# Kernel optimization log

Hardware: AMD Instinct MI355X
Metric: run time of the kernel (lower is better)

## Reference

```python
import jax, jax.numpy as jnp
import numpy as np

B, S, E, H = 8, 2048, 1024, 64

def setup_inputs() -> dict:
    key = jax.random.key(0)
    ks = jax.random.split(key, 10)
    inp = {
        'input_Q': jax.random.normal(ks[0], (B, S, E), dtype=jnp.float32),
        'input_K': jax.random.normal(ks[1], (B, S, E), dtype=jnp.float32),
        'input_V': jax.random.normal(ks[2], (B, S, E), dtype=jnp.float32),
        'mask': jax.random.randint(ks[3], (B, S, S), 0, 2) > 0,
        # Linear params: torch Linear(E, H) -> weight [H, E], use as x @ W^T + b; store transposed [E, H]
        'Wq': jax.random.normal(ks[4], (E, H), dtype=jnp.float32) / np.sqrt(E),
        'bq': jnp.zeros((H,), dtype=jnp.float32),
        'Wk': jax.random.normal(ks[5], (E, H), dtype=jnp.float32) / np.sqrt(E),
        'bk': jnp.zeros((H,), dtype=jnp.float32),
        'Wv': jax.random.normal(ks[6], (E, H), dtype=jnp.float32) / np.sqrt(E),
        'bv': jnp.zeros((H,), dtype=jnp.float32),
    }
    return inp

def reference(input_Q, input_K, input_V, mask, Wq, bq, Wk, bk, Wv, bv):
    Q = jnp.einsum('bse,eh->bsh', input_Q, Wq) + bq  # [B,S,H]
    K = jnp.einsum('bse,eh->bsh', input_K, Wk) + bk
    V = jnp.einsum('bse,eh->bsh', input_V, Wv) + bv
    scores = jnp.einsum('bqh,bkh->bqk', Q, K) / np.sqrt(H).astype(np.float32)  # [B,S,S]
    # faithful to masked_fill_(mask, 1e-10) BEFORE softmax
    scores = jnp.where(mask, jnp.float32(1e-10), scores)
    attn = jax.nn.softmax(scores, axis=-1)
    # dropout is identity in eval/reference mode
    return jnp.einsum('bqk,bkh->bqh', attn, V)
```

## Files before the change

kernel.cpp:

```cpp
#include <hip/hip_runtime.h>
#include <hip/hip_bf16.h>
#include <stdint.h>

constexpr int Bc = 8, Sc = 2048, Ec = 1024, Hc = 64;

typedef __bf16 bf16x8 __attribute__((ext_vector_type(8)));
typedef float f32x4 __attribute__((ext_vector_type(4)));
typedef unsigned short ushort8 __attribute__((ext_vector_type(8)));
typedef unsigned short ushort4v __attribute__((ext_vector_type(4)));
typedef uint32_t uint32x4 __attribute__((ext_vector_type(4)));

static __device__ __forceinline__ unsigned short f2bf(float f) {
  uint32_t u = __builtin_bit_cast(uint32_t, f);
  u = u + 0x7fffu + ((u >> 16) & 1u);
  return (unsigned short)(u >> 16);
}
static __device__ __forceinline__ bf16x8 ldb8(const unsigned short* p) {
  return __builtin_bit_cast(bf16x8, *(const ushort8*)p);
}
static __device__ __forceinline__ uint32_t pk2bf(float a, float b) {
  return (uint32_t)f2bf(a) | ((uint32_t)f2bf(b) << 16);
}

__global__ __launch_bounds__(256) void wt_kernel(
    const float* __restrict__ Wq, const float* __restrict__ Wk,
    const float* __restrict__ Wv, unsigned short* __restrict__ Wt) {
  int idx = blockIdx.x * 256 + threadIdx.x;
  int m = idx >> 16;
  int r = idx & 65535;
  int h = r >> 10;
  int e = r & 1023;
  const float* W = (m == 0) ? Wq : (m == 1) ? Wk : Wv;
  float scale = (m == 0) ? 0.125f : 1.0f;
  Wt[idx] = f2bf(W[e * Hc + h] * scale);
}

__global__ __launch_bounds__(256) void mask_kernel(
    const int* __restrict__ mask, uint32_t* __restrict__ Mb) {
  int w = blockIdx.x * 256 + threadIdx.x;
  const int* src = mask + (size_t)w * 32;
  uint32_t bits = 0;
#pragma unroll
  for (int i = 0; i < 8; i++) {
    int4 v = *(const int4*)(src + i * 4);
    bits |= (v.x ? 1u : 0u) << (i * 4 + 0);
    bits |= (v.y ? 1u : 0u) << (i * 4 + 1);
    bits |= (v.z ? 1u : 0u) << (i * 4 + 2);
    bits |= (v.w ? 1u : 0u) << (i * 4 + 3);
  }
  Mb[w] = bits;
}

__global__ __launch_bounds__(256, 5) void proj_kernel(
    const float* __restrict__ Xq, const float* __restrict__ Xk,
    const float* __restrict__ Xv, const float* __restrict__ bq,
    const float* __restrict__ bk, const float* __restrict__ bv,
    const unsigned short* __restrict__ Wt,
    unsigned short* __restrict__ Qb, unsigned short* __restrict__ Kb,
    unsigned short* __restrict__ Vt) {
  const int mat = blockIdx.y;
  const float* X = (mat == 0) ? Xq : (mat == 1) ? Xk : Xv;
  const float* bias = (mat == 0) ? bq : (mat == 1) ? bk : bv;
  const float bscale = (mat == 0) ? 0.125f : 1.0f;
  const unsigned short* W = Wt + mat * (Hc * Ec);

  const int tid = threadIdx.x;
  const int wave = tid >> 6, lane = tid & 63;
  const int rl = lane & 15, kg = lane >> 4;
  const int row0 = blockIdx.x * 16;
  const int kw = wave * 256;

  __shared__ __align__(16) char smem[32768];

  const float* xsrc = X + (size_t)row0 * Ec;
#pragma unroll
  for (int i = 0; i < 16; i++) {
    int idx = i * 256 + tid;
    float4 v = *(const float4*)(xsrc + (size_t)idx * 4);
    int f = idx * 4;
    int row = f >> 10, col = f & 1023;
    uint32_t byte = (uint32_t)(row * 2048 + col * 2) ^ (uint32_t)((row & 7) << 4);
    uint2 pk;
    pk.x = pk2bf(v.x, v.y);
    pk.y = pk2bf(v.z, v.w);
    *(uint2*)(smem + byte) = pk;
  }
  __syncthreads();

  const unsigned short* wp0 = W + (size_t)(0 * 16 + rl) * Ec + kw + kg * 8;
  const unsigned short* wp1 = W + (size_t)(1 * 16 + rl) * Ec + kw + kg * 8;
  const unsigned short* wp2 = W + (size_t)(2 * 16 + rl) * Ec + kw + kg * 8;
  const unsigned short* wp3 = W + (size_t)(3 * 16 + rl) * Ec + kw + kg * 8;

  f32x4 acc[4];
#pragma unroll
  for (int nt = 0; nt < 4; nt++) acc[nt] = (f32x4){0.f, 0.f, 0.f, 0.f};

#pragma unroll
  for (int c = 0; c < 8; c++) {
    int col = kw + kg * 8 + c * 32;
    uint32_t byte = (uint32_t)(rl * 2048 + col * 2) ^ (uint32_t)((rl & 7) << 4);
    bf16x8 aX = *(const bf16x8*)(smem + byte);
    ushort8 w0 = *(const ushort8*)(wp0 + c * 32);
    ushort8 w1 = *(const ushort8*)(wp1 + c * 32);
    ushort8 w2 = *(const ushort8*)(wp2 + c * 32);
    ushort8 w3 = *(const ushort8*)(wp3 + c * 32);
    acc[0] = __builtin_amdgcn_mfma_f32_16x16x32_bf16(
        aX, __builtin_bit_cast(bf16x8, w0), acc[0], 0, 0, 0);
    acc[1] = __builtin_amdgcn_mfma_f32_16x16x32_bf16(
        aX, __builtin_bit_cast(bf16x8, w1), acc[1], 0, 0, 0);
    acc[2] = __builtin_amdgcn_mfma_f32_16x16x32_bf16(
        aX, __builtin_bit_cast(bf16x8, w2), acc[2], 0, 0, 0);
    acc[3] = __builtin_amdgcn_mfma_f32_16x16x32_bf16(
        aX, __builtin_bit_cast(bf16x8, w3), acc[3], 0, 0, 0);
  }

  __syncthreads();
  float (*slab)[16][64] = (float (*)[16][64])smem;
#pragma unroll
  for (int nt = 0; nt < 4; nt++)
#pragma unroll
    for (int r = 0; r < 4; r++)
      slab[wave][kg * 4 + r][nt * 16 + rl] = acc[nt][r];
  __syncthreads();

  if (mat < 2) {
    unsigned short* out = (mat == 0) ? Qb : Kb;
    int row = wave * 4 + (lane >> 4);
    int col0 = (lane & 15) * 4;
    f32x4 s0 = *(const f32x4*)&slab[0][row][col0];
    f32x4 s1 = *(const f32x4*)&slab[1][row][col0];
    f32x4 s2 = *(const f32x4*)&slab[2][row][col0];
    f32x4 s3 = *(const f32x4*)&slab[3][row][col0];
    float4 bv4 = *(const float4*)(bias + col0);
    f32x4 v = s0 + s1 + s2 + s3;
    v[0] += bv4.x * bscale; v[1] += bv4.y * bscale;
    v[2] += bv4.z * bscale; v[3] += bv4.w * bscale;
    ushort4v o;
#pragma unroll
    for (int i = 0; i < 4; i++) o[i] = f2bf(v[i]);
    *(ushort4v*)(out + (size_t)(row0 + row) * Hc + col0) = o;
  } else {
    int h = lane;
    int bb = row0 >> 11;
    int sbase = (row0 & 2047) + wave * 4;
    float bh = bias[h];
    ushort4v o;
#pragma unroll
    for (int r = 0; r < 4; r++) {
      float v = slab[0][wave * 4 + r][h] + slab[1][wave * 4 + r][h] +
                slab[2][wave * 4 + r][h] + slab[3][wave * 4 + r][h] + bh;
      o[r] = f2bf(v);
    }
    *(ushort4v*)(Vt + ((size_t)bb * Hc + h) * Sc + sbase) = o;
  }
}

__global__ __launch_bounds__(256, 4) void attn_kernel(
    const unsigned short* __restrict__ Qb, const unsigned short* __restrict__ Kb,
    const unsigned short* __restrict__ Vt, const uint32_t* __restrict__ Mb,
    float* __restrict__ out) {
  const int id = blockIdx.x;
  const int b = id & 7;
  const int q0 = (id >> 3) * 16;
  const int tid = threadIdx.x;
  const int wave = tid >> 6, lane = tid & 63;
  const int rl = lane & 15;

  __shared__ unsigned short Ps[4][16][72];
  __shared__ float sm[4][16], sl[4][16];
  __shared__ float Os[4][16][64];

  const unsigned short* qptr =
      Qb + ((size_t)b * Sc + q0 + rl) * Hc + (lane >> 4) * 8;
  bf16x8 aQ0 = ldb8(qptr);
  bf16x8 aQ1 = ldb8(qptr + 32);

  float m_r[4], l_r[4];
  f32x4 Oacc[4];
#pragma unroll
  for (int r = 0; r < 4; r++) { m_r[r] = -INFINITY; l_r[r] = 0.f; }
#pragma unroll
  for (int ht = 0; ht < 4; ht++) Oacc[ht] = (f32x4){0.f, 0.f, 0.f, 0.f};

  const uint32_t* mbase[4];
#pragma unroll
  for (int r = 0; r < 4; r++)
    mbase[r] = Mb + ((size_t)b * Sc + q0 + (lane >> 4) * 4 + r) * 64;

  const unsigned short* kbase =
      Kb + ((size_t)b * Sc) * Hc + (size_t)rl * Hc + (lane >> 4) * 8;
  const unsigned short* vbase[4];
#pragma unroll
  for (int ht = 0; ht < 4; ht++)
    vbase[ht] = Vt + ((size_t)b * Hc + ht * 16 + rl) * Sc + (lane >> 4) * 8;

  const int kw = wave * 512;
  uint2 mva[4], mvb[4];

  auto issue_mask = [&](int koff, uint2 (&mv)[4]) {
#pragma unroll
    for (int r = 0; r < 4; r++)
      mv[r] = *(const uint2*)(mbase[r] + (koff >> 5));
  };
  auto compress = [&](const uint2 (&mv)[4]) -> uint32_t {
    uint32_t bits = 0;
#pragma unroll
    for (int r = 0; r < 4; r++) {
      bits |= ((mv[r].x >> rl) & 1u) << (0 + r);
      bits |= ((mv[r].x >> (16 + rl)) & 1u) << (4 + r);
      bits |= ((mv[r].y >> rl) & 1u) << (8 + r);
      bits |= ((mv[r].y >> (16 + rl)) & 1u) << (12 + r);
    }
    return bits;
  };

  auto process = [&](int koff, uint32_t bits) {
    float sv[4][4];
#pragma unroll
    for (int nt = 0; nt < 4; nt++) {
      const unsigned short* kp = kbase + (size_t)(koff + nt * 16) * Hc;
      bf16x8 bK0 = ldb8(kp);
      bf16x8 bK1 = ldb8(kp + 32);
      f32x4 s = (f32x4){0.f, 0.f, 0.f, 0.f};
      s = __builtin_amdgcn_mfma_f32_16x16x32_bf16(aQ0, bK0, s, 0, 0, 0);
      s = __builtin_amdgcn_mfma_f32_16x16x32_bf16(aQ1, bK1, s, 0, 0, 0);
#pragma unroll
      for (int r = 0; r < 4; r++)
        sv[nt][r] = ((bits >> (nt * 4 + r)) & 1u) ? 1e-10f : s[r];
    }

    float rmax[4];
#pragma unroll
    for (int r = 0; r < 4; r++) {
      rmax[r] = fmaxf(fmaxf(sv[0][r], sv[1][r]), fmaxf(sv[2][r], sv[3][r]));
#pragma unroll
      for (int off = 1; off < 16; off <<= 1)
        rmax[r] = fmaxf(rmax[r], __shfl_xor(rmax[r], off, 64));
    }

    float alpha[4], p[4][4], psum[4];
#pragma unroll
    for (int r = 0; r < 4; r++) {
      float mnew = fmaxf(m_r[r], rmax[r]);
      alpha[r] = __expf(m_r[r] - mnew);
      m_r[r] = mnew;
      psum[r] = 0.f;
    }
#pragma unroll
    for (int nt = 0; nt < 4; nt++)
#pragma unroll
      for (int r = 0; r < 4; r++) {
        p[nt][r] = __expf(sv[nt][r] - m_r[r]);
        psum[r] += p[nt][r];
      }
#pragma unroll
    for (int r = 0; r < 4; r++) {
#pragma unroll
      for (int off = 1; off < 16; off <<= 1)
        psum[r] += __shfl_xor(psum[r], off, 64);
      l_r[r] = l_r[r] * alpha[r] + psum[r];
    }
#pragma unroll
    for (int ht = 0; ht < 4; ht++)
#pragma unroll
      for (int r = 0; r < 4; r++) Oacc[ht][r] *= alpha[r];

#pragma unroll
    for (int nt = 0; nt < 4; nt++)
#pragma unroll
      for (int r = 0; r < 4; r++)
        Ps[wave][(lane >> 4) * 4 + r][nt * 16 + rl] = f2bf(p[nt][r]);

#pragma unroll
    for (int ks = 0; ks < 2; ks++) {
      bf16x8 aP = ldb8(&Ps[wave][rl][ks * 32 + (lane >> 4) * 8]);
#pragma unroll
      for (int ht = 0; ht < 4; ht++) {
        bf16x8 bV = ldb8(vbase[ht] + koff + ks * 32);
        Oacc[ht] = __builtin_amdgcn_mfma_f32_16x16x32_bf16(aP, bV, Oacc[ht], 0, 0, 0);
      }
    }
  };

  issue_mask(kw, mva);
  for (int c2 = 0; c2 < 8; c2 += 2) {
    issue_mask(kw + (c2 + 1) * 64, mvb);
    process(kw + c2 * 64, compress(mva));
    if (c2 + 2 < 8) issue_mask(kw + (c2 + 2) * 64, mva);
    process(kw + (c2 + 1) * 64, compress(mvb));
  }

  if (rl == 0) {
#pragma unroll
    for (int r = 0; r < 4; r++) {
      sm[wave][(lane >> 4) * 4 + r] = m_r[r];
      sl[wave][(lane >> 4) * 4 + r] = l_r[r];
    }
  }
  __syncthreads();

  float coef[4];
#pragma unroll
  for (int r = 0; r < 4; r++) {
    int row = (lane >> 4) * 4 + r;
    float M = fmaxf(fmaxf(sm[0][row], sm[1][row]), fmaxf(sm[2][row], sm[3][row]));
    coef[r] = __expf(m_r[r] - M);
  }
#pragma unroll
  for (int ht = 0; ht < 4; ht++)
#pragma unroll
    for (int r = 0; r < 4; r++)
      Os[wave][(lane >> 4) * 4 + r][ht * 16 + rl] = Oacc[ht][r] * coef[r];
  __syncthreads();

  {
#pragma unroll
    for (int i = 0; i < 4; i++) {
      int row = wave * 4 + i;
      float M = fmaxf(fmaxf(sm[0][row], sm[1][row]), fmaxf(sm[2][row], sm[3][row]));
      float L = sl[0][row] * __expf(sm[0][row] - M) +
                sl[1][row] * __expf(sm[1][row] - M) +
                sl[2][row] * __expf(sm[2][row] - M) +
                sl[3][row] * __expf(sm[3][row] - M);
      float acc = Os[0][row][lane] + Os[1][row][lane] +
                  Os[2][row][lane] + Os[3][row][lane];
      out[((size_t)b * Sc + q0 + row) * Hc + lane] = acc / L;
    }
  }
}

extern "C" void kernel_launch(void* const* d_in, const int* in_sizes, int n_in,
                              void* d_out, int out_size, void* d_ws, size_t ws_size,
                              hipStream_t stream) {
  const float* Xq = (const float*)d_in[0];
  const float* Xk = (const float*)d_in[1];
  const float* Xv = (const float*)d_in[2];
  const int* mask = (const int*)d_in[3];
  const float* Wq = (const float*)d_in[4];
  const float* bq = (const float*)d_in[5];
  const float* Wk = (const float*)d_in[6];
  const float* bk = (const float*)d_in[7];
  const float* Wv = (const float*)d_in[8];
  const float* bv = (const float*)d_in[9];

  unsigned short* Qb = (unsigned short*)d_ws;
  unsigned short* Kb = Qb + (size_t)Bc * Sc * Hc;
  unsigned short* Vt = Kb + (size_t)Bc * Sc * Hc;
  unsigned short* Wt = Vt + (size_t)Bc * Sc * Hc;
  uint32_t* Mb = (uint32_t*)(Wt + (size_t)3 * Hc * Ec);

  wt_kernel<<<dim3(3 * Hc * Ec / 256), 256, 0, stream>>>(Wq, Wk, Wv, Wt);
  mask_kernel<<<dim3(Bc * Sc * (Sc / 32) / 256), 256, 0, stream>>>(mask, Mb);
  proj_kernel<<<dim3(Bc * Sc / 16, 3), 256, 0, stream>>>(Xq, Xk, Xv, bq, bk, bv,
                                                         Wt, Qb, Kb, Vt);
  attn_kernel<<<dim3(Bc * Sc / 16), 256, 0, stream>>>(Qb, Kb, Vt, Mb,
                                                      (float*)d_out);
}
```

Baseline: 424.3 us.

## Pipeline projection X loads via direct global-to-LDS double buffering

Rewrites the projection kernel so each block processes 64 rows as four 16-row slabs. Raw fp32 X is streamed directly into LDS with global_load_lds in a double-buffered pipeline, and the bf16 conversion moves into the compute step. Each wave now owns 16 output columns over the full K dimension, which removes the cross-wave LDS reduction. The cost is a smaller grid, 64KB of LDS per block, and hand-placed waitcnt/barrier synchronisation that is fragile.

```diff
diff --git a/kernel.cpp b/kernel.cpp
--- a/kernel.cpp
+++ b/kernel.cpp
@@ -21,6 +21,11 @@
 static __device__ __forceinline__ uint32_t pk2bf(float a, float b) {
   return (uint32_t)f2bf(a) | ((uint32_t)f2bf(b) << 16);
 }
+
+#define GLOBAL_LOAD_LDS16(g, l)                                              \
+  __builtin_amdgcn_global_load_lds(                                          \
+      (const __attribute__((address_space(1))) void*)(g),                    \
+      (__attribute__((address_space(3))) void*)(l), 16, 0, 0)
 
 __global__ __launch_bounds__(256) void wt_kernel(
     const float* __restrict__ Wq, const float* __restrict__ Wk,
@@ -51,7 +56,7 @@
   Mb[w] = bits;
 }
 
-__global__ __launch_bounds__(256, 5) void proj_kernel(
+__global__ __launch_bounds__(256, 2) void proj_kernel(
     const float* __restrict__ Xq, const float* __restrict__ Xk,
     const float* __restrict__ Xv, const float* __restrict__ bq,
     const float* __restrict__ bk, const float* __restrict__ bv,
@@ -67,92 +72,89 @@
   const int tid = threadIdx.x;
   const int wave = tid >> 6, lane = tid & 63;
   const int rl = lane & 15, kg = lane >> 4;
-  const int row0 = blockIdx.x * 16;
-  const int kw = wave * 256;
-
-  __shared__ __align__(16) char smem[32768];
-
-  const float* xsrc = X + (size_t)row0 * Ec;
-#pragma unroll
-  for (int i = 0; i < 16; i++) {
-    int idx = i * 256 + tid;
-    float4 v = *(const float4*)(xsrc + (size_t)idx * 4);
-    int f = idx * 4;
-    int row = f >> 10, col = f & 1023;
-    uint32_t byte = (uint32_t)(row * 2048 + col * 2) ^ (uint32_t)((row & 7) << 4);
-    uint2 pk;
-    pk.x = pk2bf(v.x, v.y);
-    pk.y = pk2bf(v.z, v.w);
-    *(uint2*)(smem + byte) = pk;
-  }
-  __syncthreads();
-
-  const unsigned short* wp0 = W + (size_t)(0 * 16 + rl) * Ec + kw + kg * 8;
-  const unsigned short* wp1 = W + (size_t)(1 * 16 + rl) * Ec + kw + kg * 8;
-  const unsigned short* wp2 = W + (size_t)(2 * 16 + rl) * Ec + kw + kg * 8;
-  const unsigned short* wp3 = W + (size_t)(3 * 16 + rl) * Ec + kw + kg * 8;
-
-  f32x4 acc[4];
-#pragma unroll
-  for (int nt = 0; nt < 4; nt++) acc[nt] = (f32x4){0.f, 0.f, 0.f, 0.f};
-
-#pragma unroll
-  for (int c = 0; c < 8; c++) {
-    int col = kw + kg * 8 + c * 32;
-    uint32_t byte = (uint32_t)(rl * 2048 + col * 2) ^ (uint32_t)((rl & 7) << 4);
-    bf16x8 aX = *(const bf16x8*)(smem + byte);
-    ushort8 w0 = *(const ushort8*)(wp0 + c * 32);
-    ushort8 w1 = *(const ushort8*)(wp1 + c * 32);
-    ushort8 w2 = *(const ushort8*)(wp2 + c * 32);
-    ushort8 w3 = *(const ushort8*)(wp3 + c * 32);
-    acc[0] = __builtin_amdgcn_mfma_f32_16x16x32_bf16(
-        aX, __builtin_bit_cast(bf16x8, w0), acc[0], 0, 0, 0);
-    acc[1] = __builtin_amdgcn_mfma_f32_16x16x32_bf16(
-        aX, __builtin_bit_cast(bf16x8, w1), acc[1], 0, 0, 0);
-    acc[2] = __builtin_amdgcn_mfma_f32_16x16x32_bf16(
-        aX, __builtin_bit_cast(bf16x8, w2), acc[2], 0, 0, 0);
-    acc[3] = __builtin_amdgcn_mfma_f32_16x16x32_bf16(
-        aX, __builtin_bit_cast(bf16x8, w3), acc[3], 0, 0, 0);
-  }
-
-  __syncthreads();
-  float (*slab)[16][64] = (float (*)[16][64])smem;
-#pragma unroll
-  for (int nt = 0; nt < 4; nt++)
-#pragma unroll
-    for (int r = 0; r < 4; r++)
-      slab[wave][kg * 4 + r][nt * 16 + rl] = acc[nt][r];
-  __syncthreads();
-
-  if (mat < 2) {
-    unsigned short* out = (mat == 0) ? Qb : Kb;
-    int row = wave * 4 + (lane >> 4);
-    int col0 = (lane & 15) * 4;
-    f32x4 s0 = *(const f32x4*)&slab[0][row][col0];
-    f32x4 s1 = *(const f32x4*)&slab[1][row][col0];
-    f32x4 s2 = *(const f32x4*)&slab[2][row][col0];
-    f32x4 s3 = *(const f32x4*)&slab[3][row][col0];
-    float4 bv4 = *(const float4*)(bias + col0);
-    f32x4 v = s0 + s1 + s2 + s3;
-    v[0] += bv4.x * bscale; v[1] += bv4.y * bscale;
-    v[2] += bv4.z * bscale; v[3] += bv4.w * bscale;
-    ushort4v o;
-#pragma unroll
-    for (int i = 0; i < 4; i++) o[i] = f2bf(v[i]);
-    *(ushort4v*)(out + (size_t)(row0 + row) * Hc + col0) = o;
-  } else {
-    int h = lane;
-    int bb = row0 >> 11;
-    int sbase = (row0 & 2047) + wave * 4;
-    float bh = bias[h];
-    ushort4v o;
-#pragma unroll
-    for (int r = 0; r < 4; r++) {
-      float v = slab[0][wave * 4 + r][h] + slab[1][wave * 4 + r][h] +
-                slab[2][wave * 4 + r][h] + slab[3][wave * 4 + r][h] + bh;
-      o[r] = f2bf(v);
-    }
-    *(ushort4v*)(Vt + ((size_t)bb * Hc + h) * Sc + sbase) = o;
+
+  __shared__ __align__(16) char smem[65536];
+
+  const char* xb = (const char*)X + (size_t)blockIdx.x * 262144;
+  const unsigned short* wp_base = W + (size_t)(wave * 16 + rl) * Ec + kg * 8;
+  const float bcol = bias[wave * 16 + rl] * bscale;
+
+  auto stage = [&](int slab, int half, int buf) {
+#pragma unroll
+    for (int j = 0; j < 8; j++) {
+      int row = wave * 4 + (j >> 1);
+      int part = j & 1;
+      const char* src = xb + (size_t)slab * 65536 + row * 4096 + half * 2048 +
+                        part * 1024 + ((lane ^ (row & 7)) * 16);
+      char* dst = smem + buf * 32768 + row * 2048 + part * 1024;
+      GLOBAL_LOAD_LDS16(src, dst);
+    }
+  };
+
+  auto compute = [&](int half, int buf, f32x4& acc) {
+    const char* lb = smem + buf * 32768;
+    const unsigned short* wp = wp_base + half * 512;
+    const uint32_t sw = (uint32_t)((rl & 7) << 4);
+#pragma unroll
+    for (int c = 0; c < 16; c++) {
+      uint32_t boff = (uint32_t)(kg * 32 + c * 128);
+      float4 x0 = *(const float4*)(lb + rl * 2048 + (boff ^ sw));
+      float4 x1 = *(const float4*)(lb + rl * 2048 + ((boff + 16) ^ sw));
+      ushort8 wv = *(const ushort8*)(wp + c * 32);
+      uint32x4 u = (uint32x4){pk2bf(x0.x, x0.y), pk2bf(x0.z, x0.w),
+                              pk2bf(x1.x, x1.y), pk2bf(x1.z, x1.w)};
+      acc = __builtin_amdgcn_mfma_f32_16x16x32_bf16(
+          __builtin_bit_cast(bf16x8, u), __builtin_bit_cast(bf16x8, wv), acc,
+          0, 0, 0);
+    }
+  };
+
+  stage(0, 0, 0);
+  stage(0, 1, 1);
+
+#pragma unroll 1
+  for (int sl = 0; sl < 4; sl++) {
+    f32x4 acc = (f32x4){0.f, 0.f, 0.f, 0.f};
+
+    asm volatile("s_waitcnt vmcnt(8)" ::: "memory");
+    __builtin_amdgcn_sched_barrier(0);
+    __builtin_amdgcn_s_barrier();
+    compute(0, 0, acc);
+    asm volatile("s_waitcnt lgkmcnt(0)" ::: "memory");
+    __builtin_amdgcn_sched_barrier(0);
+    __builtin_amdgcn_s_barrier();
+    if (sl < 3) stage(sl + 1, 0, 0);
+
+    if (sl < 3)
+      asm volatile("s_waitcnt vmcnt(8)" ::: "memory");
+    else
+      asm volatile("s_waitcnt vmcnt(0)" ::: "memory");
+    __builtin_amdgcn_sched_barrier(0);
+    __builtin_amdgcn_s_barrier();
+    compute(1, 1, acc);
+
+    {
+      int rowg = blockIdx.x * 64 + sl * 16;
+      if (mat < 2) {
+        unsigned short* out = (mat == 0) ? Qb : Kb;
+#pragma unroll
+        for (int r = 0; r < 4; r++)
+          out[(size_t)(rowg + kg * 4 + r) * Hc + wave * 16 + rl] =
+              f2bf(acc[r] + bcol);
+      } else {
+        int bb = rowg >> 11;
+        int sloc = (rowg & 2047) + kg * 4;
+        ushort4v o;
+#pragma unroll
+        for (int r = 0; r < 4; r++) o[r] = f2bf(acc[r] + bcol);
+        *(ushort4v*)(Vt + ((size_t)bb * Hc + wave * 16 + rl) * Sc + sloc) = o;
+      }
+    }
+
+    asm volatile("s_waitcnt lgkmcnt(0)" ::: "memory");
+    __builtin_amdgcn_sched_barrier(0);
+    __builtin_amdgcn_s_barrier();
+    if (sl < 3) stage(sl + 1, 1, 1);
   }
 }
 
@@ -352,8 +354,8 @@
 
   wt_kernel<<<dim3(3 * Hc * Ec / 256), 256, 0, stream>>>(Wq, Wk, Wv, Wt);
   mask_kernel<<<dim3(Bc * Sc * (Sc / 32) / 256), 256, 0, stream>>>(mask, Mb);
-  proj_kernel<<<dim3(Bc * Sc / 16, 3), 256, 0, stream>>>(Xq, Xk, Xv, bq, bk, bv,
-                                                         Wt, Qb, Kb, Vt);
+  proj_kernel<<<dim3(256, 3), 256, 0, stream>>>(Xq, Xk, Xv, bq, bk, bv,
+                                                Wt, Qb, Kb, Vt);
   attn_kernel<<<dim3(Bc * Sc / 16), 256, 0, stream>>>(Qb, Kb, Vt, Mb,
                                                       (float*)d_out);
 }
```

Result: slower. 436.0 us (+2.8%).

## Prefetch K tiles across chunks, add MFMA priority hints, split projection launches

Applied to the files above, without the earlier changes.

The attention kernel now double-buffers K operand loads in registers, issuing the next chunk's K loads right after the current QK^T MFMAs so their latency overlaps the softmax work. MFMA sections are wrapped in s_setprio to favour matrix issue across waves. The projection kernel is split into three separate launches with scalar arguments instead of one 2D grid that selects pointers per block. The prefetch raises register pressure, which may lower occupancy, and the extra launches add launch overhead.

```diff
diff --git a/kernel.cpp b/kernel.cpp
--- a/kernel.cpp
+++ b/kernel.cpp
@@ -52,18 +52,9 @@
 }
 
 __global__ __launch_bounds__(256, 5) void proj_kernel(
-    const float* __restrict__ Xq, const float* __restrict__ Xk,
-    const float* __restrict__ Xv, const float* __restrict__ bq,
-    const float* __restrict__ bk, const float* __restrict__ bv,
-    const unsigned short* __restrict__ Wt,
-    unsigned short* __restrict__ Qb, unsigned short* __restrict__ Kb,
-    unsigned short* __restrict__ Vt) {
-  const int mat = blockIdx.y;
-  const float* X = (mat == 0) ? Xq : (mat == 1) ? Xk : Xv;
-  const float* bias = (mat == 0) ? bq : (mat == 1) ? bk : bv;
-  const float bscale = (mat == 0) ? 0.125f : 1.0f;
-  const unsigned short* W = Wt + mat * (Hc * Ec);
-
+    const float* __restrict__ X, const float* __restrict__ bias,
+    const unsigned short* __restrict__ W, unsigned short* __restrict__ out,
+    float bscale, int vmode) {
   const int tid = threadIdx.x;
   const int wave = tid >> 6, lane = tid & 63;
   const int rl = lane & 15, kg = lane >> 4;
@@ -124,8 +115,7 @@
       slab[wave][kg * 4 + r][nt * 16 + rl] = acc[nt][r];
   __syncthreads();
 
-  if (mat < 2) {
-    unsigned short* out = (mat == 0) ? Qb : Kb;
+  if (vmode == 0) {
     int row = wave * 4 + (lane >> 4);
     int col0 = (lane & 15) * 4;
     f32x4 s0 = *(const f32x4*)&slab[0][row][col0];
@@ -152,7 +142,7 @@
                 slab[2][wave * 4 + r][h] + slab[3][wave * 4 + r][h] + bh;
       o[r] = f2bf(v);
     }
-    *(ushort4v*)(Vt + ((size_t)bb * Hc + h) * Sc + sbase) = o;
+    *(ushort4v*)(out + ((size_t)bb * Hc + h) * Sc + sbase) = o;
   }
 }
 
@@ -197,6 +187,7 @@
 
   const int kw = wave * 512;
   uint2 mva[4], mvb[4];
+  bf16x8 kA[4][2], kB[4][2];
 
   auto issue_mask = [&](int koff, uint2 (&mv)[4]) {
 #pragma unroll
@@ -214,21 +205,31 @@
     }
     return bits;
   };
-
-  auto process = [&](int koff, uint32_t bits) {
-    float sv[4][4];
+  auto loadK = [&](int koff, bf16x8 (&kb)[4][2]) {
 #pragma unroll
     for (int nt = 0; nt < 4; nt++) {
       const unsigned short* kp = kbase + (size_t)(koff + nt * 16) * Hc;
-      bf16x8 bK0 = ldb8(kp);
-      bf16x8 bK1 = ldb8(kp + 32);
+      kb[nt][0] = ldb8(kp);
+      kb[nt][1] = ldb8(kp + 32);
+    }
+  };
+
+  auto process = [&](int koff, uint32_t bits, const bf16x8 (&kb)[4][2],
+                     bool pre, int koff_next, bf16x8 (&knext)[4][2]) {
+    float sv[4][4];
+    __builtin_amdgcn_s_setprio(1);
+#pragma unroll
+    for (int nt = 0; nt < 4; nt++) {
       f32x4 s = (f32x4){0.f, 0.f, 0.f, 0.f};
-      s = __builtin_amdgcn_mfma_f32_16x16x32_bf16(aQ0, bK0, s, 0, 0, 0);
-      s = __builtin_amdgcn_mfma_f32_16x16x32_bf16(aQ1, bK1, s, 0, 0, 0);
+      s = __builtin_amdgcn_mfma_f32_16x16x32_bf16(aQ0, kb[nt][0], s, 0, 0, 0);
+      s = __builtin_amdgcn_mfma_f32_16x16x32_bf16(aQ1, kb[nt][1], s, 0, 0, 0);
 #pragma unroll
       for (int r = 0; r < 4; r++)
         sv[nt][r] = ((bits >> (nt * 4 + r)) & 1u) ? 1e-10f : s[r];
     }
+    __builtin_amdgcn_s_setprio(0);
+
+    if (pre) loadK(koff_next, knext);
 
     float rmax[4];
 #pragma unroll
@@ -272,6 +273,7 @@
       for (int r = 0; r < 4; r++)
         Ps[wave][(lane >> 4) * 4 + r][nt * 16 + rl] = f2bf(p[nt][r]);
 
+    __builtin_amdgcn_s_setprio(1);
 #pragma unroll
     for (int ks = 0; ks < 2; ks++) {
       bf16x8 aP = ldb8(&Ps[wave][rl][ks * 32 + (lane >> 4) * 8]);
@@ -281,14 +283,17 @@
         Oacc[ht] = __builtin_amdgcn_mfma_f32_16x16x32_bf16(aP, bV, Oacc[ht], 0, 0, 0);
       }
     }
+    __builtin_amdgcn_s_setprio(0);
   };
 
+  loadK(kw, kA);
   issue_mask(kw, mva);
   for (int c2 = 0; c2 < 8; c2 += 2) {
     issue_mask(kw + (c2 + 1) * 64, mvb);
-    process(kw + c2 * 64, compress(mva));
+    process(kw + c2 * 64, compress(mva), kA, true, kw + (c2 + 1) * 64, kB);
     if (c2 + 2 < 8) issue_mask(kw + (c2 + 2) * 64, mva);
-    process(kw + (c2 + 1) * 64, compress(mvb));
+    process(kw + (c2 + 1) * 64, compress(mvb), kB, c2 + 2 < 8,
+            kw + (c2 + 2) * 64, kA);
   }
 
   if (rl == 0) {
@@ -352,8 +357,11 @@
 
   wt_kernel<<<dim3(3 * Hc * Ec / 256), 256, 0, stream>>>(Wq, Wk, Wv, Wt);
   mask_kernel<<<dim3(Bc * Sc * (Sc / 32) / 256), 256, 0, stream>>>(mask, Mb);
-  proj_kernel<<<dim3(Bc * Sc / 16, 3), 256, 0, stream>>>(Xq, Xk, Xv, bq, bk, bv,
-                                                         Wt, Qb, Kb, Vt);
+  proj_kernel<<<dim3(Bc * Sc / 16), 256, 0, stream>>>(Xq, bq, Wt, Qb, 0.125f, 0);
+  proj_kernel<<<dim3(Bc * Sc / 16), 256, 0, stream>>>(Xk, bk, Wt + (size_t)Hc * Ec,
+                                                      Kb, 1.0f, 0);
+  proj_kernel<<<dim3(Bc * Sc / 16), 256, 0, stream>>>(Xv, bv, Wt + (size_t)2 * Hc * Ec,
+                                                      Vt, 1.0f, 1);
   attn_kernel<<<dim3(Bc * Sc / 16), 256, 0, stream>>>(Qb, Kb, Vt, Mb,
                                                       (float*)d_out);
 }
```

Result: slower. 466.9 us (+10.0%).
